# Kernel optimization log

Measured on AMD Instinct MI355X. Metric: run time of the kernel, lower is better.

## Reference

```python
import jax, jax.numpy as jnp
import numpy as np

B, D, P, C = 4096, 512, 256, 8
LAMBDA = 1.0


def setup_inputs() -> dict:
    key = jax.random.key(0)
    k1, k2, k3, k4 = jax.random.split(key, 4)
    x = jax.random.normal(k1, (B, D), dtype=jnp.float32)
    y = jax.random.randint(k2, (B,), 0, C, dtype=jnp.int32)
    prototypes = jax.random.normal(k3, (P, D), dtype=jnp.float32)
    # omega initialized as eye + 0.01*randn per class, like the torch module
    omega = jnp.eye(D, dtype=jnp.float32)[None] + 0.01 * jax.random.normal(k4, (C, D, D), dtype=jnp.float32)
    prototype_labels = (jnp.arange(P, dtype=jnp.int32) % C).astype(jnp.int32)
    return {"x": x, "y": y, "prototypes": prototypes, "omega": omega, "prototype_labels": prototype_labels}


def reference(x, y, prototypes, omega, prototype_labels):
    # transformed inputs per class: tx[c,b,:] = omega[c] @ x[b]
    tx = jnp.einsum('cij,bj->cbi', omega, x)                     # [C,B,D]
    # transformed prototypes under every class omega, then pick each
    # prototype's own class matrix: tp[p,:] = omega[label[p]] @ w[p]
    tp_all = jnp.einsum('cij,pj->cpi', omega, prototypes)        # [C,P,D]
    tp = tp_all[prototype_labels, jnp.arange(P)]                 # [P,D]
    # squared distances via expansion ||a-b||^2 = |a|^2 + |b|^2 - 2ab
    dots = jnp.einsum('cbd,pd->cbp', tx, tp)                     # [C,B,P]
    x2 = jnp.sum(tx * tx, axis=-1)                               # [C,B]
    p2 = jnp.sum(tp * tp, axis=-1)                               # [P]
    dist_all = x2[:, :, None] + p2[None, None, :] - 2.0 * dots   # [C,B,P]
    # each prototype uses the omega of its own class
    dist = dist_all[prototype_labels, :, jnp.arange(P)].T        # [B,P]
    same = prototype_labels[None, :] == y[:, None]               # [B,P]
    inf = jnp.float32(jnp.inf)
    pos = jnp.min(jnp.where(same, dist, inf), axis=1)            # [B]
    neg = jnp.min(jnp.where(same, inf, dist), axis=1)            # [B]
    mu = (pos - neg) / (pos + neg)
    loss = jnp.mean(jax.nn.sigmoid(LAMBDA * mu))
    loss = loss + 0.01 * jnp.linalg.norm(omega.reshape(-1))
    return loss
```

## Files before the change

kernel.cpp:

```cpp
#include <hip/hip_runtime.h>
#include <math.h>

typedef unsigned short ushort_t;
typedef __attribute__((ext_vector_type(8))) short short8;
typedef __attribute__((ext_vector_type(4))) float f32x4;

#define B_N 4096
#define D_N 512
#define P_N 256
#define C_N 8

#define ACC_OFF   0
#define P2G_OFF   256
#define X2_OFF    1280
#define XB_OFF    132352
#define OMB_OFF   (XB_OFF + B_N*D_N*2)
#define TPG_OFF   (OMB_OFF + C_N*D_N*D_N*2)
#define UG_OFF    (TPG_OFF + P_N*D_N*2)
#define OMBT_OFF  (UG_OFF + P_N*D_N*2)
#define MINB_OFF  OMBT_OFF

#define MFMA16(a, b, c) __builtin_amdgcn_mfma_f32_16x16x32_bf16(a, b, c, 0, 0, 0)

__device__ inline ushort_t f2bf(float f) {
    union { float f; unsigned u; } v; v.f = f;
    unsigned r = v.u + 0x7FFFu + ((v.u >> 16) & 1u);
    return (ushort_t)(r >> 16);
}

__device__ __forceinline__ void gll16(const ushort_t* g, ushort_t* l) {
    __builtin_amdgcn_global_load_lds((const __attribute__((address_space(1))) void*)g,
                                     (__attribute__((address_space(3))) void*)l, 16, 0, 0);
}

__global__ void k_cast_x(const float* __restrict__ x, ushort_t* __restrict__ xb) {
    int idx = blockIdx.x * 256 + threadIdx.x;
    const float4* x4 = (const float4*)x;
    float4 a = x4[idx * 2], b = x4[idx * 2 + 1];
    union { ushort_t s[8]; uint4 v; } o;
    o.s[0] = f2bf(a.x); o.s[1] = f2bf(a.y); o.s[2] = f2bf(a.z); o.s[3] = f2bf(a.w);
    o.s[4] = f2bf(b.x); o.s[5] = f2bf(b.y); o.s[6] = f2bf(b.z); o.s[7] = f2bf(b.w);
    ((uint4*)xb)[idx] = o.v;
}

__global__ void k_cast_om(const float* __restrict__ omega, ushort_t* __restrict__ omb,
                          ushort_t* __restrict__ ombT, float* __restrict__ oss) {
    int c = blockIdx.z, r0 = blockIdx.y * 64, c0 = blockIdx.x * 64;
    __shared__ ushort_t T[64][72];
    __shared__ float red[4];
    int t = threadIdx.x;
    int r = t >> 2, seg = t & 3;
    const float* src = omega + ((size_t)c * D_N + r0 + r) * D_N + c0 + seg * 16;
    float4 v0 = ((const float4*)src)[0], v1 = ((const float4*)src)[1];
    float4 v2 = ((const float4*)src)[2], v3 = ((const float4*)src)[3];
    float s = v0.x*v0.x + v0.y*v0.y + v0.z*v0.z + v0.w*v0.w
            + v1.x*v1.x + v1.y*v1.y + v1.z*v1.z + v1.w*v1.w
            + v2.x*v2.x + v2.y*v2.y + v2.z*v2.z + v2.w*v2.w
            + v3.x*v3.x + v3.y*v3.y + v3.z*v3.z + v3.w*v3.w;
    union { ushort_t s[16]; uint4 v[2]; } o;
    float vv[16] = {v0.x,v0.y,v0.z,v0.w, v1.x,v1.y,v1.z,v1.w,
                    v2.x,v2.y,v2.z,v2.w, v3.x,v3.y,v3.z,v3.w};
    #pragma unroll
    for (int j = 0; j < 16; ++j) o.s[j] = f2bf(vv[j]);
    uint4* dst = (uint4*)(omb + ((size_t)c * D_N + r0 + r) * D_N + c0 + seg * 16);
    dst[0] = o.v[0]; dst[1] = o.v[1];
    #pragma unroll
    for (int j = 0; j < 16; ++j) T[seg * 16 + j][r] = o.s[j];
    __syncthreads();
    int jr = t >> 2, sg2 = t & 3;
    uint4 w0 = *(uint4*)&T[jr][sg2 * 16];
    uint4 w1 = *(uint4*)&T[jr][sg2 * 16 + 8];
    uint4* dstT = (uint4*)(ombT + ((size_t)c * D_N + c0 + jr) * D_N + r0 + sg2 * 16);
    dstT[0] = w0; dstT[1] = w1;
    #pragma unroll
    for (int off = 32; off > 0; off >>= 1) s += __shfl_down(s, off);
    if ((t & 63) == 0) red[t >> 6] = s;
    __syncthreads();
    if (t == 0) atomicAdd(oss, red[0] + red[1] + red[2] + red[3]);
}

__global__ __launch_bounds__(256) void k_tp(const float* __restrict__ prot,
                                            const ushort_t* __restrict__ omb,
                                            ushort_t* __restrict__ tpg,
                                            float* __restrict__ p2g) {
    int i0 = blockIdx.x * 64, c = blockIdx.y;
    __shared__ ushort_t As[32][72];
    __shared__ ushort_t Bs[64][72];
    int t = threadIdx.x, w = t >> 6, lane = t & 63;
    int g = lane >> 4, cl = lane & 15;
    f32x4 acc[2] = {{0,0,0,0},{0,0,0,0}};
    for (int k0 = 0; k0 < D_N; k0 += 64) {
        __syncthreads();
        {
            int m = t >> 3, seg = t & 7;
            const float* ap = prot + ((size_t)(c + 8 * m)) * D_N + k0 + seg * 8;
            float4 u0 = ((const float4*)ap)[0], u1 = ((const float4*)ap)[1];
            union { ushort_t s[8]; uint4 v; } o;
            o.s[0]=f2bf(u0.x); o.s[1]=f2bf(u0.y); o.s[2]=f2bf(u0.z); o.s[3]=f2bf(u0.w);
            o.s[4]=f2bf(u1.x); o.s[5]=f2bf(u1.y); o.s[6]=f2bf(u1.z); o.s[7]=f2bf(u1.w);
            *(uint4*)&As[m][seg * 8] = o.v;
        }
        {
            int r = t >> 2, sg = t & 3;
            const uint4* bp = (const uint4*)(omb + ((size_t)c * D_N + i0 + r) * D_N + k0 + sg * 16);
            *(uint4*)&Bs[r][sg * 16] = bp[0];
            *(uint4*)&Bs[r][sg * 16 + 8] = bp[1];
        }
        __syncthreads();
        #pragma unroll
        for (int kk = 0; kk < 2; ++kk) {
            int koff = kk * 32 + g * 8;
            short8 bfr = *(const short8*)&Bs[w * 16 + cl][koff];
            #pragma unroll
            for (int mt = 0; mt < 2; ++mt) {
                short8 afr = *(const short8*)&As[mt * 16 + cl][koff];
                acc[mt] = MFMA16(afr, bfr, acc[mt]);
            }
        }
    }
    #pragma unroll
    for (int mt = 0; mt < 2; ++mt)
        #pragma unroll
        for (int reg = 0; reg < 4; ++reg) {
            float v = acc[mt][reg];
            int m = mt * 16 + g * 4 + reg;
            int i = i0 + w * 16 + cl;
            tpg[((size_t)c * 32 + m) * D_N + i] = f2bf(v);
            float s = v * v;
            s += __shfl_xor(s, 1); s += __shfl_xor(s, 2);
            s += __shfl_xor(s, 4); s += __shfl_xor(s, 8);
            if (cl == 0) atomicAdd(&p2g[c * 32 + m], s);
        }
}

__global__ __launch_bounds__(256) void k_u(const ushort_t* __restrict__ tpg,
                                           const ushort_t* __restrict__ ombT,
                                           ushort_t* __restrict__ ug) {
    int j0 = blockIdx.x * 64, c = blockIdx.y;
    __shared__ ushort_t As[32][72];
    __shared__ ushort_t Bs[64][72];
    int t = threadIdx.x, w = t >> 6, lane = t & 63;
    int g = lane >> 4, cl = lane & 15;
    f32x4 acc[2] = {{0,0,0,0},{0,0,0,0}};
    for (int k0 = 0; k0 < D_N; k0 += 64) {
        __syncthreads();
        {
            int m = t >> 3, seg = t & 7;
            *(uint4*)&As[m][seg * 8] =
                *(const uint4*)(tpg + ((size_t)c * 32 + m) * D_N + k0 + seg * 8);
        }
        {
            int r = t >> 2, sg = t & 3;
            const uint4* bp = (const uint4*)(ombT + ((size_t)c * D_N + j0 + r) * D_N + k0 + sg * 16);
            *(uint4*)&Bs[r][sg * 16] = bp[0];
            *(uint4*)&Bs[r][sg * 16 + 8] = bp[1];
        }
        __syncthreads();
        #pragma unroll
        for (int kk = 0; kk < 2; ++kk) {
            int koff = kk * 32 + g * 8;
            short8 bfr = *(const short8*)&Bs[w * 16 + cl][koff];
            #pragma unroll
            for (int mt = 0; mt < 2; ++mt) {
                short8 afr = *(const short8*)&As[mt * 16 + cl][koff];
                acc[mt] = MFMA16(afr, bfr, acc[mt]);
            }
        }
    }
    #pragma unroll
    for (int mt = 0; mt < 2; ++mt)
        #pragma unroll
        for (int reg = 0; reg < 4; ++reg) {
            int m = mt * 16 + g * 4 + reg;
            int j = j0 + w * 16 + cl;
            ug[((size_t)c * 32 + m) * D_N + j] = f2bf(acc[mt][reg]);
        }
}

__global__ __launch_bounds__(256, 4) void k_x2d(const ushort_t* __restrict__ xb,
                                                const ushort_t* __restrict__ omb,
                                                const ushort_t* __restrict__ ug,
                                                const float* __restrict__ p2g,
                                                float* __restrict__ x2,
                                                float* __restrict__ minb) {
    int c  = blockIdx.y;
    int b0 = blockIdx.z * 128;
    int t = threadIdx.x, w = t >> 6, lane = t & 63;
    int g = lane >> 4, cl = lane & 15;
    int srow = lane >> 2, spos = lane & 3;

    __shared__ ushort_t Xs[2][128][32];
    __shared__ ushort_t Os[2][128][32];
    __shared__ float red[128][2];

    if (blockIdx.x < 4) {
        int i0 = blockIdx.x * 128;
        int qr = w >> 1, qc = w & 1;
        f32x4 acc[4][4];
        #pragma unroll
        for (int mt = 0; mt < 4; ++mt)
            #pragma unroll
            for (int nt = 0; nt < 4; ++nt) acc[mt][nt] = (f32x4){0,0,0,0};
        #pragma unroll
        for (int i = 0; i < 2; ++i) {
            int rb = w * 32 + i * 16;
            int r  = rb + srow;
            int cg = (spos + r) & 3;
            gll16(xb + (size_t)(b0 + r) * D_N + cg * 8, &Xs[0][rb][0]);
            gll16(omb + ((size_t)c * D_N + i0 + r) * D_N + cg * 8, &Os[0][rb][0]);
        }
        __syncthreads();
        for (int s = 0; s < 16; ++s) {
            int cb = s & 1, nb = cb ^ 1;
            if (s < 15) {
                int k1 = (s + 1) * 32;
                #pragma unroll
                for (int i = 0; i < 2; ++i) {
                    int rb = w * 32 + i * 16;
                    int r  = rb + srow;
                    int cg = (spos + r) & 3;
                    gll16(xb + (size_t)(b0 + r) * D_N + k1 + cg * 8, &Xs[nb][rb][0]);
                    gll16(omb + ((size_t)c * D_N + i0 + r) * D_N + k1 + cg * 8, &Os[nb][rb][0]);
                }
            }
            short8 a[4], b[4];
            #pragma unroll
            for (int mt = 0; mt < 4; ++mt) {
                int r = qr * 64 + mt * 16 + cl;
                a[mt] = *(const short8*)&Xs[cb][r][((g - r) & 3) * 8];
            }
            #pragma unroll
            for (int nt = 0; nt < 4; ++nt) {
                int r = qc * 64 + nt * 16 + cl;
                b[nt] = *(const short8*)&Os[cb][r][((g - r) & 3) * 8];
            }
            #pragma unroll
            for (int mt = 0; mt < 4; ++mt)
                #pragma unroll
                for (int nt = 0; nt < 4; ++nt)
                    acc[mt][nt] = MFMA16(a[mt], b[nt], acc[mt][nt]);
            __syncthreads();
        }
        #pragma unroll
        for (int mt = 0; mt < 4; ++mt)
            #pragma unroll
            for (int reg = 0; reg < 4; ++reg) {
                float s = 0.f;
                #pragma unroll
                for (int nt = 0; nt < 4; ++nt) s += acc[mt][nt][reg] * acc[mt][nt][reg];
                s += __shfl_xor(s, 1); s += __shfl_xor(s, 2);
                s += __shfl_xor(s, 4); s += __shfl_xor(s, 8);
                if (cl == 0) red[qr * 64 + mt * 16 + g * 4 + reg][qc] = s;
            }
        __syncthreads();
        if (t < 128) atomicAdd(&x2[(size_t)(b0 + t) * C_N + c], red[t][0] + red[t][1]);
    } else {
        f32x4 acc[2][2];
        #pragma unroll
        for (int mt = 0; mt < 2; ++mt)
            #pragma unroll
            for (int nt = 0; nt < 2; ++nt) acc[mt][nt] = (f32x4){0,0,0,0};
        #pragma unroll
        for (int i = 0; i < 2; ++i) {
            int rb = w * 32 + i * 16;
            int r  = rb + srow;
            int cg = (spos + r) & 3;
            gll16(xb + (size_t)(b0 + r) * D_N + cg * 8, &Xs[0][rb][0]);
        }
        if (w < 2) {
            int rb = w * 16;
            int r  = rb + srow;
            int cg = (spos + r) & 3;
            gll16(ug + ((size_t)c * 32 + r) * D_N + cg * 8, &Os[0][rb][0]);
        }
        __syncthreads();
        for (int s = 0; s < 16; ++s) {
            int cb = s & 1, nb = cb ^ 1;
            if (s < 15) {
                int k1 = (s + 1) * 32;
                #pragma unroll
                for (int i = 0; i < 2; ++i) {
                    int rb = w * 32 + i * 16;
                    int r  = rb + srow;
                    int cg = (spos + r) & 3;
                    gll16(xb + (size_t)(b0 + r) * D_N + k1 + cg * 8, &Xs[nb][rb][0]);
                }
                if (w < 2) {
                    int rb = w * 16;
                    int r  = rb + srow;
                    int cg = (spos + r) & 3;
                    gll16(ug + ((size_t)c * 32 + r) * D_N + k1 + cg * 8, &Os[nb][rb][0]);
                }
            }
            short8 a[2], b[2];
            #pragma unroll
            for (int mt = 0; mt < 2; ++mt) {
                int r = w * 32 + mt * 16 + cl;
                a[mt] = *(const short8*)&Xs[cb][r][((g - r) & 3) * 8];
            }
            #pragma unroll
            for (int nt = 0; nt < 2; ++nt) {
                int r = nt * 16 + cl;
                b[nt] = *(const short8*)&Os[cb][r][((g - r) & 3) * 8];
            }
            #pragma unroll
            for (int mt = 0; mt < 2; ++mt)
                #pragma unroll
                for (int nt = 0; nt < 2; ++nt)
                    acc[mt][nt] = MFMA16(a[mt], b[nt], acc[mt][nt]);
            __syncthreads();
        }
        #pragma unroll
        for (int mt = 0; mt < 2; ++mt)
            #pragma unroll
            for (int reg = 0; reg < 4; ++reg) {
                float v = INFINITY;
                #pragma unroll
                for (int nt = 0; nt < 2; ++nt) {
                    int q = c * 32 + nt * 16 + cl;
                    v = fminf(v, p2g[q] - 2.f * acc[mt][nt][reg]);
                }
                v = fminf(v, __shfl_xor(v, 1)); v = fminf(v, __shfl_xor(v, 2));
                v = fminf(v, __shfl_xor(v, 4)); v = fminf(v, __shfl_xor(v, 8));
                if (cl == 0)
                    minb[(size_t)(b0 + w * 32 + mt * 16 + g * 4 + reg) * C_N + c] = v;
            }
    }
}

__global__ void k_mu(const float* __restrict__ x2, const float* __restrict__ minb,
                     const int* __restrict__ y, float* __restrict__ acc) {
    int t = threadIdx.x;
    int b = blockIdx.x * 256 + t;
    int yb = y[b];
    float d[8];
    #pragma unroll
    for (int cc = 0; cc < 8; ++cc)
        d[cc] = x2[(size_t)b * C_N + cc] + minb[(size_t)b * C_N + cc];
    float pos = d[yb];
    float neg = INFINITY;
    #pragma unroll
    for (int cc = 0; cc < 8; ++cc)
        if (cc != yb) neg = fminf(neg, d[cc]);
    float mu = (pos - neg) / (pos + neg);
    float s = 1.f / (1.f + expf(-mu));
    #pragma unroll
    for (int off = 32; off > 0; off >>= 1) s += __shfl_down(s, off);
    __shared__ float red[4];
    if ((t & 63) == 0) red[t >> 6] = s;
    __syncthreads();
    if (t == 0) atomicAdd(acc, red[0] + red[1] + red[2] + red[3]);
}

__global__ void k_final(const float* __restrict__ accs, float* __restrict__ out) {
    out[0] = accs[0] * (1.f / (float)B_N) + 0.01f * sqrtf(accs[1]);
}

extern "C" void kernel_launch(void* const* d_in, const int* in_sizes, int n_in,
                              void* d_out, int out_size, void* d_ws, size_t ws_size,
                              hipStream_t stream) {
    (void)in_sizes; (void)n_in; (void)out_size; (void)ws_size;
    const float* x     = (const float*)d_in[0];
    const int*   y     = (const int*)d_in[1];
    const float* prot  = (const float*)d_in[2];
    const float* omega = (const float*)d_in[3];

    char* ws = (char*)d_ws;
    float*    accs = (float*)(ws + ACC_OFF);
    float*    p2g  = (float*)(ws + P2G_OFF);
    float*    x2   = (float*)(ws + X2_OFF);
    ushort_t* xb   = (ushort_t*)(ws + XB_OFF);
    ushort_t* omb  = (ushort_t*)(ws + OMB_OFF);
    ushort_t* tpg  = (ushort_t*)(ws + TPG_OFF);
    ushort_t* ug   = (ushort_t*)(ws + UG_OFF);
    ushort_t* ombT = (ushort_t*)(ws + OMBT_OFF);
    float*    minb = (float*)(ws + MINB_OFF);

    (void)hipMemsetAsync(ws, 0, XB_OFF, stream);
    k_cast_x <<<B_N * D_N / 8 / 256, 256, 0, stream>>>(x, xb);
    k_cast_om<<<dim3(8, 8, C_N), 256, 0, stream>>>(omega, omb, ombT, accs + 1);
    k_tp     <<<dim3(8, C_N), 256, 0, stream>>>(prot, omb, tpg, p2g);
    k_u      <<<dim3(8, C_N), 256, 0, stream>>>(tpg, ombT, ug);
    k_x2d    <<<dim3(5, C_N, B_N / 128), 256, 0, stream>>>(xb, omb, ug, p2g, x2, minb);
    k_mu     <<<B_N / 256, 256, 0, stream>>>(x2, minb, y, accs);
    k_final  <<<1, 1, 0, stream>>>(accs, (float*)d_out);
}
```

Before: 135.4 us.

## Fuse cast kernels, precompute Gram matrix, add swizzle, fold finalization into distance kernel

Merges the x and omega cast kernels into one launch. Replaces the two chained prototype GEMMs with a per-class Gram matrix G = omega^T omega followed by a single prototype-times-G GEMM. p2 is now taken as w·(Gw). Changes the LDS swizzle in the distance kernel to reduce bank conflicts, and replaces the mu and final kernels with a last-block reduction at the end of the distance kernel. Computing G adds a large new GEMM (C×D×D×D) and stores it in bf16, which also changes the rounding of p2. In exchange the change removes launches and one dependent GEMM stage.

```diff
diff --git a/kernel.cpp b/kernel.cpp
--- a/kernel.cpp
+++ b/kernel.cpp
@@ -14,11 +14,11 @@
 #define P2G_OFF   256
 #define X2_OFF    1280
 #define XB_OFF    132352
-#define OMB_OFF   (XB_OFF + B_N*D_N*2)
-#define TPG_OFF   (OMB_OFF + C_N*D_N*D_N*2)
-#define UG_OFF    (TPG_OFF + P_N*D_N*2)
-#define OMBT_OFF  (UG_OFF + P_N*D_N*2)
-#define MINB_OFF  OMBT_OFF
+#define OMB_OFF   (XB_OFF  + B_N*D_N*2)
+#define OMBT_OFF  (OMB_OFF + C_N*D_N*D_N*2)
+#define GB_OFF    (OMBT_OFF+ C_N*D_N*D_N*2)
+#define UG_OFF    (GB_OFF  + C_N*D_N*D_N*2)
+#define MINB_OFF  GB_OFF
 
 #define MFMA16(a, b, c) __builtin_amdgcn_mfma_f32_16x16x32_bf16(a, b, c, 0, 0, 0)
 
@@ -33,22 +33,24 @@
                                      (__attribute__((address_space(3))) void*)l, 16, 0, 0);
 }
 
-__global__ void k_cast_x(const float* __restrict__ x, ushort_t* __restrict__ xb) {
-    int idx = blockIdx.x * 256 + threadIdx.x;
-    const float4* x4 = (const float4*)x;
-    float4 a = x4[idx * 2], b = x4[idx * 2 + 1];
-    union { ushort_t s[8]; uint4 v; } o;
-    o.s[0] = f2bf(a.x); o.s[1] = f2bf(a.y); o.s[2] = f2bf(a.z); o.s[3] = f2bf(a.w);
-    o.s[4] = f2bf(b.x); o.s[5] = f2bf(b.y); o.s[6] = f2bf(b.z); o.s[7] = f2bf(b.w);
-    ((uint4*)xb)[idx] = o.v;
-}
-
-__global__ void k_cast_om(const float* __restrict__ omega, ushort_t* __restrict__ omb,
-                          ushort_t* __restrict__ ombT, float* __restrict__ oss) {
-    int c = blockIdx.z, r0 = blockIdx.y * 64, c0 = blockIdx.x * 64;
+__global__ void k_cast(const float* __restrict__ x, const float* __restrict__ omega,
+                       ushort_t* __restrict__ xb, ushort_t* __restrict__ omb,
+                       ushort_t* __restrict__ ombT, float* __restrict__ oss) {
     __shared__ ushort_t T[64][72];
     __shared__ float red[4];
     int t = threadIdx.x;
+    if (blockIdx.x < 1024) {
+        int idx = blockIdx.x * 256 + t;
+        const float4* x4 = (const float4*)x;
+        float4 a = x4[idx * 2], b = x4[idx * 2 + 1];
+        union { ushort_t s[8]; uint4 v; } o;
+        o.s[0] = f2bf(a.x); o.s[1] = f2bf(a.y); o.s[2] = f2bf(a.z); o.s[3] = f2bf(a.w);
+        o.s[4] = f2bf(b.x); o.s[5] = f2bf(b.y); o.s[6] = f2bf(b.z); o.s[7] = f2bf(b.w);
+        ((uint4*)xb)[idx] = o.v;
+        return;
+    }
+    int bb = blockIdx.x - 1024;
+    int c = bb >> 6, r0 = ((bb >> 3) & 7) * 64, c0 = (bb & 7) * 64;
     int r = t >> 2, seg = t & 3;
     const float* src = omega + ((size_t)c * D_N + r0 + r) * D_N + c0 + seg * 16;
     float4 v0 = ((const float4*)src)[0], v1 = ((const float4*)src)[1];
@@ -79,11 +81,65 @@
     if (t == 0) atomicAdd(oss, red[0] + red[1] + red[2] + red[3]);
 }
 
-__global__ __launch_bounds__(256) void k_tp(const float* __restrict__ prot,
-                                            const ushort_t* __restrict__ omb,
-                                            ushort_t* __restrict__ tpg,
+__global__ __launch_bounds__(256) void k_G(const ushort_t* __restrict__ ombT,
+                                           ushort_t* __restrict__ Gb) {
+    int i0 = blockIdx.x * 64, j0 = blockIdx.y * 64, c = blockIdx.z;
+    __shared__ ushort_t As[64][72];
+    __shared__ ushort_t Bs[64][72];
+    int t = threadIdx.x, w = t >> 6, lane = t & 63;
+    int qr = w >> 1, qc = w & 1;
+    int g = lane >> 4, cl = lane & 15;
+    f32x4 acc[2][2];
+    #pragma unroll
+    for (int mt = 0; mt < 2; ++mt)
+        #pragma unroll
+        for (int nt = 0; nt < 2; ++nt) acc[mt][nt] = (f32x4){0,0,0,0};
+    for (int k0 = 0; k0 < D_N; k0 += 64) {
+        __syncthreads();
+        {
+            int r = t >> 2, sg = t & 3;
+            const uint4* ap = (const uint4*)(ombT + ((size_t)c * D_N + i0 + r) * D_N + k0 + sg * 16);
+            *(uint4*)&As[r][sg * 16] = ap[0];
+            *(uint4*)&As[r][sg * 16 + 8] = ap[1];
+            const uint4* bp = (const uint4*)(ombT + ((size_t)c * D_N + j0 + r) * D_N + k0 + sg * 16);
+            *(uint4*)&Bs[r][sg * 16] = bp[0];
+            *(uint4*)&Bs[r][sg * 16 + 8] = bp[1];
+        }
+        __syncthreads();
+        #pragma unroll
+        for (int kk = 0; kk < 2; ++kk) {
+            int koff = kk * 32 + g * 8;
+            short8 a[2], b[2];
+            #pragma unroll
+            for (int mt = 0; mt < 2; ++mt)
+                a[mt] = *(const short8*)&As[qr * 32 + mt * 16 + cl][koff];
+            #pragma unroll
+            for (int nt = 0; nt < 2; ++nt)
+                b[nt] = *(const short8*)&Bs[qc * 32 + nt * 16 + cl][koff];
+            #pragma unroll
+            for (int mt = 0; mt < 2; ++mt)
+                #pragma unroll
+                for (int nt = 0; nt < 2; ++nt)
+                    acc[mt][nt] = MFMA16(a[mt], b[nt], acc[mt][nt]);
+        }
+    }
+    #pragma unroll
+    for (int mt = 0; mt < 2; ++mt)
+        #pragma unroll
+        for (int nt = 0; nt < 2; ++nt)
+            #pragma unroll
+            for (int reg = 0; reg < 4; ++reg) {
+                int i = i0 + qr * 32 + mt * 16 + g * 4 + reg;
+                int j = j0 + qc * 32 + nt * 16 + cl;
+                Gb[((size_t)c * D_N + i) * D_N + j] = f2bf(acc[mt][nt][reg]);
+            }
+}
+
+__global__ __launch_bounds__(256) void k_u2(const float* __restrict__ prot,
+                                            const ushort_t* __restrict__ Gb,
+                                            ushort_t* __restrict__ ug,
                                             float* __restrict__ p2g) {
-    int i0 = blockIdx.x * 64, c = blockIdx.y;
+    int j0 = blockIdx.x * 64, c = blockIdx.y;
     __shared__ ushort_t As[32][72];
     __shared__ ushort_t Bs[64][72];
     int t = threadIdx.x, w = t >> 6, lane = t & 63;
@@ -102,7 +158,7 @@
         }
         {
             int r = t >> 2, sg = t & 3;
-            const uint4* bp = (const uint4*)(omb + ((size_t)c * D_N + i0 + r) * D_N + k0 + sg * 16);
+            const uint4* bp = (const uint4*)(Gb + ((size_t)c * D_N + j0 + r) * D_N + k0 + sg * 16);
             *(uint4*)&Bs[r][sg * 16] = bp[0];
             *(uint4*)&Bs[r][sg * 16 + 8] = bp[1];
         }
@@ -124,56 +180,12 @@
         for (int reg = 0; reg < 4; ++reg) {
             float v = acc[mt][reg];
             int m = mt * 16 + g * 4 + reg;
-            int i = i0 + w * 16 + cl;
-            tpg[((size_t)c * 32 + m) * D_N + i] = f2bf(v);
-            float s = v * v;
+            int j = j0 + w * 16 + cl;
+            ug[((size_t)c * 32 + m) * D_N + j] = f2bf(v);
+            float s = prot[((size_t)(c + 8 * m)) * D_N + j] * v;
             s += __shfl_xor(s, 1); s += __shfl_xor(s, 2);
             s += __shfl_xor(s, 4); s += __shfl_xor(s, 8);
             if (cl == 0) atomicAdd(&p2g[c * 32 + m], s);
-        }
-}
-
-__global__ __launch_bounds__(256) void k_u(const ushort_t* __restrict__ tpg,
-                                           const ushort_t* __restrict__ ombT,
-                                           ushort_t* __restrict__ ug) {
-    int j0 = blockIdx.x * 64, c = blockIdx.y;
-    __shared__ ushort_t As[32][72];
-    __shared__ ushort_t Bs[64][72];
-    int t = threadIdx.x, w = t >> 6, lane = t & 63;
-    int g = lane >> 4, cl = lane & 15;
-    f32x4 acc[2] = {{0,0,0,0},{0,0,0,0}};
-    for (int k0 = 0; k0 < D_N; k0 += 64) {
-        __syncthreads();
-        {
-            int m = t >> 3, seg = t & 7;
-            *(uint4*)&As[m][seg * 8] =
-                *(const uint4*)(tpg + ((size_t)c * 32 + m) * D_N + k0 + seg * 8);
-        }
-        {
-            int r = t >> 2, sg = t & 3;
-            const uint4* bp = (const uint4*)(ombT + ((size_t)c * D_N + j0 + r) * D_N + k0 + sg * 16);
-            *(uint4*)&Bs[r][sg * 16] = bp[0];
-            *(uint4*)&Bs[r][sg * 16 + 8] = bp[1];
-        }
-        __syncthreads();
-        #pragma unroll
-        for (int kk = 0; kk < 2; ++kk) {
-            int koff = kk * 32 + g * 8;
-            short8 bfr = *(const short8*)&Bs[w * 16 + cl][koff];
-            #pragma unroll
-            for (int mt = 0; mt < 2; ++mt) {
-                short8 afr = *(const short8*)&As[mt * 16 + cl][koff];
-                acc[mt] = MFMA16(afr, bfr, acc[mt]);
-            }
-        }
-    }
-    #pragma unroll
-    for (int mt = 0; mt < 2; ++mt)
-        #pragma unroll
-        for (int reg = 0; reg < 4; ++reg) {
-            int m = mt * 16 + g * 4 + reg;
-            int j = j0 + w * 16 + cl;
-            ug[((size_t)c * 32 + m) * D_N + j] = f2bf(acc[mt][reg]);
         }
 }
 
@@ -182,7 +194,10 @@
                                                 const ushort_t* __restrict__ ug,
                                                 const float* __restrict__ p2g,
                                                 float* __restrict__ x2,
-                                                float* __restrict__ minb) {
+                                                float* __restrict__ minb,
+                                                const int* __restrict__ y,
+                                                float* __restrict__ accs,
+                                                float* __restrict__ out) {
     int c  = blockIdx.y;
     int b0 = blockIdx.z * 128;
     int t = threadIdx.x, w = t >> 6, lane = t & 63;
@@ -192,6 +207,8 @@
     __shared__ ushort_t Xs[2][128][32];
     __shared__ ushort_t Os[2][128][32];
     __shared__ float red[128][2];
+    __shared__ float red2[4];
+    __shared__ int slast;
 
     if (blockIdx.x < 4) {
         int i0 = blockIdx.x * 128;
@@ -205,7 +222,7 @@
         for (int i = 0; i < 2; ++i) {
             int rb = w * 32 + i * 16;
             int r  = rb + srow;
-            int cg = (spos + r) & 3;
+            int cg = (spos + r + (r >> 2)) & 3;
             gll16(xb + (size_t)(b0 + r) * D_N + cg * 8, &Xs[0][rb][0]);
             gll16(omb + ((size_t)c * D_N + i0 + r) * D_N + cg * 8, &Os[0][rb][0]);
         }
@@ -218,7 +235,7 @@
                 for (int i = 0; i < 2; ++i) {
                     int rb = w * 32 + i * 16;
                     int r  = rb + srow;
-                    int cg = (spos + r) & 3;
+                    int cg = (spos + r + (r >> 2)) & 3;
                     gll16(xb + (size_t)(b0 + r) * D_N + k1 + cg * 8, &Xs[nb][rb][0]);
                     gll16(omb + ((size_t)c * D_N + i0 + r) * D_N + k1 + cg * 8, &Os[nb][rb][0]);
                 }
@@ -227,12 +244,12 @@
             #pragma unroll
             for (int mt = 0; mt < 4; ++mt) {
                 int r = qr * 64 + mt * 16 + cl;
-                a[mt] = *(const short8*)&Xs[cb][r][((g - r) & 3) * 8];
+                a[mt] = *(const short8*)&Xs[cb][r][((g - r - (r >> 2)) & 3) * 8];
             }
             #pragma unroll
             for (int nt = 0; nt < 4; ++nt) {
                 int r = qc * 64 + nt * 16 + cl;
-                b[nt] = *(const short8*)&Os[cb][r][((g - r) & 3) * 8];
+                b[nt] = *(const short8*)&Os[cb][r][((g - r - (r >> 2)) & 3) * 8];
             }
             #pragma unroll
             for (int mt = 0; mt < 4; ++mt)
@@ -264,13 +281,13 @@
         for (int i = 0; i < 2; ++i) {
             int rb = w * 32 + i * 16;
             int r  = rb + srow;
-            int cg = (spos + r) & 3;
+            int cg = (spos + r + (r >> 2)) & 3;
             gll16(xb + (size_t)(b0 + r) * D_N + cg * 8, &Xs[0][rb][0]);
         }
         if (w < 2) {
             int rb = w * 16;
             int r  = rb + srow;
-            int cg = (spos + r) & 3;
+            int cg = (spos + r + (r >> 2)) & 3;
             gll16(ug + ((size_t)c * 32 + r) * D_N + cg * 8, &Os[0][rb][0]);
         }
         __syncthreads();
@@ -282,13 +299,13 @@
                 for (int i = 0; i < 2; ++i) {
                     int rb = w * 32 + i * 16;
                     int r  = rb + srow;
-                    int cg = (spos + r) & 3;
+                    int cg = (spos + r + (r >> 2)) & 3;
                     gll16(xb + (size_t)(b0 + r) * D_N + k1 + cg * 8, &Xs[nb][rb][0]);
                 }
                 if (w < 2) {
                     int rb = w * 16;
                     int r  = rb + srow;
-                    int cg = (spos + r) & 3;
+                    int cg = (spos + r + (r >> 2)) & 3;
                     gll16(ug + ((size_t)c * 32 + r) * D_N + k1 + cg * 8, &Os[nb][rb][0]);
                 }
             }
@@ -296,12 +313,12 @@
             #pragma unroll
             for (int mt = 0; mt < 2; ++mt) {
                 int r = w * 32 + mt * 16 + cl;
-                a[mt] = *(const short8*)&Xs[cb][r][((g - r) & 3) * 8];
+                a[mt] = *(const short8*)&Xs[cb][r][((g - r - (r >> 2)) & 3) * 8];
             }
             #pragma unroll
             for (int nt = 0; nt < 2; ++nt) {
                 int r = nt * 16 + cl;
-                b[nt] = *(const short8*)&Os[cb][r][((g - r) & 3) * 8];
+                b[nt] = *(const short8*)&Os[cb][r][((g - r - (r >> 2)) & 3) * 8];
             }
             #pragma unroll
             for (int mt = 0; mt < 2; ++mt)
@@ -326,34 +343,36 @@
                     minb[(size_t)(b0 + w * 32 + mt * 16 + g * 4 + reg) * C_N + c] = v;
             }
     }
-}
-
-__global__ void k_mu(const float* __restrict__ x2, const float* __restrict__ minb,
-                     const int* __restrict__ y, float* __restrict__ acc) {
-    int t = threadIdx.x;
-    int b = blockIdx.x * 256 + t;
-    int yb = y[b];
-    float d[8];
-    #pragma unroll
-    for (int cc = 0; cc < 8; ++cc)
-        d[cc] = x2[(size_t)b * C_N + cc] + minb[(size_t)b * C_N + cc];
-    float pos = d[yb];
-    float neg = INFINITY;
-    #pragma unroll
-    for (int cc = 0; cc < 8; ++cc)
-        if (cc != yb) neg = fminf(neg, d[cc]);
-    float mu = (pos - neg) / (pos + neg);
-    float s = 1.f / (1.f + expf(-mu));
-    #pragma unroll
-    for (int off = 32; off > 0; off >>= 1) s += __shfl_down(s, off);
-    __shared__ float red[4];
-    if ((t & 63) == 0) red[t >> 6] = s;
+
+    __threadfence();
+    if (t == 0)
+        slast = (atomicAdd((unsigned*)accs + 2, 1u) == 5u * C_N * (B_N / 128) - 1u);
     __syncthreads();
-    if (t == 0) atomicAdd(acc, red[0] + red[1] + red[2] + red[3]);
-}
-
-__global__ void k_final(const float* __restrict__ accs, float* __restrict__ out) {
-    out[0] = accs[0] * (1.f / (float)B_N) + 0.01f * sqrtf(accs[1]);
+    if (slast) {
+        __threadfence();
+        float local = 0.f;
+        for (int b = t; b < B_N; b += 256) {
+            int yb = y[b];
+            float pd[8];
+            #pragma unroll
+            for (int cc = 0; cc < 8; ++cc)
+                pd[cc] = x2[(size_t)b * C_N + cc] + minb[(size_t)b * C_N + cc];
+            float pos = pd[yb];
+            float neg = INFINITY;
+            #pragma unroll
+            for (int cc = 0; cc < 8; ++cc)
+                if (cc != yb) neg = fminf(neg, pd[cc]);
+            float mu = (pos - neg) / (pos + neg);
+            local += 1.f / (1.f + expf(-mu));
+        }
+        #pragma unroll
+        for (int off = 32; off > 0; off >>= 1) local += __shfl_down(local, off);
+        if ((t & 63) == 0) red2[t >> 6] = local;
+        __syncthreads();
+        if (t == 0)
+            out[0] = (red2[0] + red2[1] + red2[2] + red2[3]) * (1.f / (float)B_N)
+                   + 0.01f * sqrtf(accs[1]);
+    }
 }
 
 extern "C" void kernel_launch(void* const* d_in, const int* in_sizes, int n_in,
@@ -371,17 +390,15 @@
     float*    x2   = (float*)(ws + X2_OFF);
     ushort_t* xb   = (ushort_t*)(ws + XB_OFF);
     ushort_t* omb  = (ushort_t*)(ws + OMB_OFF);
-    ushort_t* tpg  = (ushort_t*)(ws + TPG_OFF);
+    ushort_t* ombT = (ushort_t*)(ws + OMBT_OFF);
+    ushort_t* Gb   = (ushort_t*)(ws + GB_OFF);
     ushort_t* ug   = (ushort_t*)(ws + UG_OFF);
-    ushort_t* ombT = (ushort_t*)(ws + OMBT_OFF);
     float*    minb = (float*)(ws + MINB_OFF);
 
     (void)hipMemsetAsync(ws, 0, XB_OFF, stream);
-    k_cast_x <<<B_N * D_N / 8 / 256, 256, 0, stream>>>(x, xb);
-    k_cast_om<<<dim3(8, 8, C_N), 256, 0, stream>>>(omega, omb, ombT, accs + 1);
-    k_tp     <<<dim3(8, C_N), 256, 0, stream>>>(prot, omb, tpg, p2g);
-    k_u      <<<dim3(8, C_N), 256, 0, stream>>>(tpg, ombT, ug);
-    k_x2d    <<<dim3(5, C_N, B_N / 128), 256, 0, stream>>>(xb, omb, ug, p2g, x2, minb);
-    k_mu     <<<B_N / 256, 256, 0, stream>>>(x2, minb, y, accs);
-    k_final  <<<1, 1, 0, stream>>>(accs, (float*)d_out);
-}
+    k_cast<<<1536, 256, 0, stream>>>(x, omega, xb, omb, ombT, accs + 1);
+    k_G   <<<dim3(8, 8, C_N), 256, 0, stream>>>(ombT, Gb);
+    k_u2  <<<dim3(8, C_N), 256, 0, stream>>>(prot, Gb, ug, p2g);
+    k_x2d <<<dim3(5, C_N, B_N / 128), 256, 0, stream>>>(xb, omb, ug, p2g, x2, minb,
+                                                        y, accs, (float*)d_out);
+}
```

After: 227.1 us. 1.68x slower.
